# Performance work log

Measured on AMD Instinct MI355X. Metric: run time of the kernel, lower is better.

Reference implementation:

```python
import jax, jax.numpy as jnp
import numpy as np

H = 16  # attention heads


def setup_inputs() -> dict:
    key = jax.random.key(0)
    k0, k1, k2 = jax.random.split(key, 3)
    B, T, C = 2, 2048, 1024
    x = jax.random.normal(k0, (B, T, C), dtype=jnp.float32)
    W_attn = jax.random.normal(k1, (3 * C, C), dtype=jnp.float32) * 0.02
    W_proj = jax.random.normal(k2, (C, C), dtype=jnp.float32) * 0.02
    b_proj = jnp.zeros((C,), dtype=jnp.float32)
    return {"x": x, "W_attn": W_attn, "W_proj": W_proj, "b_proj": b_proj}


def reference(x, W_attn, W_proj, b_proj):
    # Eval-mode (dropout = identity), rotational_embeddings=False, flash=False path.
    B, T, C = x.shape
    d = C // H
    qkv = jnp.einsum('btc,fc->btf', x, W_attn)          # [B,T,3C] fused QKV proj
    q, k, v = jnp.split(qkv, 3, axis=-1)
    # [B,T,C] -> [B,H,T,d]
    q = q.reshape(B, T, H, d).transpose(0, 2, 1, 3)
    k = k.reshape(B, T, H, d).transpose(0, 2, 1, 3)
    v = v.reshape(B, T, H, d).transpose(0, 2, 1, 3)
    scale = 1.0 / np.sqrt(d).astype(np.float32)
    att = jnp.einsum('bhqd,bhkd->bhqk', q, k) * scale    # full TxT scores (no mask)
    att = jax.nn.softmax(att, axis=-1)
    y = jnp.einsum('bhqk,bhkd->bhqd', att, v)            # [B,H,T,d]
    y = y.transpose(0, 2, 1, 3).reshape(B, T, C)
    return jnp.einsum('btc,oc->bto', y, W_proj) + b_proj
```

## Files before the change

### kernel.cpp

```cpp
#include <hip/hip_runtime.h>
#include <hip/hip_bf16.h>
#include <stdint.h>

typedef __attribute__((ext_vector_type(8))) short bf16x8;
typedef __attribute__((ext_vector_type(4))) float f32x4;
typedef __attribute__((ext_vector_type(4))) unsigned u32x4;

#define MFMA16(A,B,C) __builtin_amdgcn_mfma_f32_16x16x32_bf16(A,B,C,0,0,0)


__device__ inline void gld_lds16(const __hip_bfloat16* g, __hip_bfloat16* l) {
  __builtin_amdgcn_global_load_lds(
      (const __attribute__((address_space(1))) void*)g,
      (__attribute__((address_space(3))) void*)l, 16, 0, 0);
}

__device__ inline void cvt_store8r(float4 u0, float4 u1,
                                   __hip_bfloat16* __restrict__ l) {
  __hip_bfloat162 t[4];
  t[0] = __float22bfloat162_rn(float2{u0.x, u0.y});
  t[1] = __float22bfloat162_rn(float2{u0.z, u0.w});
  t[2] = __float22bfloat162_rn(float2{u1.x, u1.y});
  t[3] = __float22bfloat162_rn(float2{u1.z, u1.w});
  *(int4*)l = *(const int4*)t;
}

__device__ inline void comb_store8r(int4 av, int4 bv, float rinv,
                                    __hip_bfloat16* __restrict__ l) {
  const __hip_bfloat162* ap = (const __hip_bfloat162*)&av;
  const __hip_bfloat162* bp = (const __hip_bfloat162*)&bv;
  __hip_bfloat162 t[4];
#pragma unroll
  for (int i = 0; i < 4; i++) {
    float2 fa = __bfloat1622float2(ap[i]);
    float2 fb = __bfloat1622float2(bp[i]);
    t[i] = __float22bfloat162_rn(float2{(fa.x + fb.x) * rinv,
                                        (fa.y + fb.y) * rinv});
  }
  *(int4*)l = *(const int4*)t;
}

__device__ inline unsigned pkbf(float a, float b) {
  __hip_bfloat162 t = __float22bfloat162_rn(float2{a, b});
  return *(unsigned*)&t;
}

__device__ inline void quad_mix(unsigned &a, unsigned &b) {
#if __has_builtin(__builtin_amdgcn_permlane32_swap) && __has_builtin(__builtin_amdgcn_permlane16_swap)
  auto r1 = __builtin_amdgcn_permlane32_swap(a, b, false, false);
  auto r2 = __builtin_amdgcn_permlane16_swap(r1[0], r1[1], false, false);
  a = r2[0];
  b = r2[1];
#else
  int lane = (int)(threadIdx.x & 63);
  int g = lane >> 4;
  int lm = lane & 15;
  int slo = (((g << 1) & 3) << 4) | lm;
  int shi = ((((g << 1) | 1) & 3) << 4) | lm;
  unsigned t0 = (unsigned)__shfl((int)a, slo, 64);
  unsigned t1 = (unsigned)__shfl((int)b, slo, 64);
  unsigned t2 = (unsigned)__shfl((int)a, shi, 64);
  unsigned t3 = (unsigned)__shfl((int)b, shi, 64);
  bool hi = g >= 2;
  unsigned na = hi ? t1 : t0;
  unsigned nb = hi ? t3 : t2;
  a = na;
  b = nb;
#endif
}

__global__ __launch_bounds__(256)
void gemm_qkv(const float* __restrict__ A,
              const float* __restrict__ B,
              __hip_bfloat16* __restrict__ C,
              __hip_bfloat16* __restrict__ vtg,
              int M, int N, int K)
{
  __shared__ __align__(16) __hip_bfloat16 As[128 * 32];
  __shared__ __align__(16) __hip_bfloat16 Bs[128 * 32];

  const int tid  = threadIdx.x;
  const int lane = tid & 63;
  const int w    = tid >> 6;
  const int lm   = lane & 15;
  const int g    = lane >> 4;

  const int bm = blockIdx.y * 128;
  const int bn = blockIdx.x * 128;
  const int rm = (w >> 1) * 64;
  const int cn = (w & 1) * 64;

  const int row0 = tid >> 2;
  const int kc   = (tid & 3) * 8;

  float4 pa[2][2], pb[2][2];
  auto ldtile = [&](int k0) {
#pragma unroll
    for (int p = 0; p < 2; p++) {
      const float* ga = A + (size_t)(bm + row0 + 64 * p) * K + k0 + kc;
      pa[p][0] = *(const float4*)ga;
      pa[p][1] = *(const float4*)(ga + 4);
      const float* gb = B + (size_t)(bn + row0 + 64 * p) * K + k0 + kc;
      pb[p][0] = *(const float4*)gb;
      pb[p][1] = *(const float4*)(gb + 4);
    }
  };

  const f32x4 fzero = {0.0f, 0.0f, 0.0f, 0.0f};
  f32x4 acc[4][4];
  for (int i = 0; i < 4; i++)
    for (int j = 0; j < 4; j++)
      acc[i][j] = fzero;

  ldtile(0);
  for (int k0 = 0; k0 < K; k0 += 32) {
#pragma unroll
    for (int p = 0; p < 2; p++) {
      int row = row0 + 64 * p;
      cvt_store8r(pa[p][0], pa[p][1], &As[row * 32 + kc]);
      cvt_store8r(pb[p][0], pb[p][1], &Bs[row * 32 + kc]);
    }
    __syncthreads();
    if (k0 + 32 < K) ldtile(k0 + 32);

    bf16x8 af[4], bfr[4];
#pragma unroll
    for (int i = 0; i < 4; i++)
      af[i] = *(const bf16x8*)&As[(rm + 16 * i + lm) * 32 + 8 * g];
#pragma unroll
    for (int j = 0; j < 4; j++)
      bfr[j] = *(const bf16x8*)&Bs[(cn + 16 * j + lm) * 32 + 8 * g];
#pragma unroll
    for (int i = 0; i < 4; i++)
#pragma unroll
      for (int j = 0; j < 4; j++)
        acc[i][j] = MFMA16(af[i], bfr[j], acc[i][j]);
    __syncthreads();
  }

  if (bn >= 2048) {
#pragma unroll
    for (int j = 0; j < 4; j++) {
      int colv = bn + cn + 16 * j + lm - 2048;
      int vh = colv >> 6, dd = colv & 63;
#pragma unroll
      for (int i = 0; i < 4; i++) {
        int m0 = bm + rm + 16 * i + 4 * g;
        int bb = m0 >> 11, t0 = m0 & 2047;
        __hip_bfloat16 t4[4];
#pragma unroll
        for (int r = 0; r < 4; r++) t4[r] = __float2bfloat16(acc[i][j][r]);
        *(int2*)&vtg[((size_t)(bb * 16 + vh) * 64 + dd) * 2048 + t0] =
            *(const int2*)t4;
      }
    }
    return;
  }

  const float qs = (bn < 1024) ? (0.125f * 1.4426950408889634f) : 1.0f;
#pragma unroll
  for (int j = 0; j < 4; j++) {
    int coln = bn + cn + 16 * j + lm;
#pragma unroll
    for (int i = 0; i < 4; i++) {
#pragma unroll
      for (int r = 0; r < 4; r++) {
        int rowm = bm + rm + 16 * i + 4 * g + r;
        C[(size_t)rowm * N + coln] = __float2bfloat16(acc[i][j][r] * qs);
      }
    }
  }
}

__global__ __launch_bounds__(256)
void gemm_out(const __hip_bfloat16* __restrict__ po,
              const float* __restrict__ pl,
              const float* __restrict__ Bw,
              const float* __restrict__ bias,
              float* __restrict__ out,
              int M, int N, int K)
{
  __shared__ __align__(16) __hip_bfloat16 As[128 * 32];
  __shared__ __align__(16) __hip_bfloat16 Bs[64 * 32];

  const int tid  = threadIdx.x;
  const int lane = tid & 63;
  const int w    = tid >> 6;
  const int lm   = lane & 15;
  const int g    = lane >> 4;

  const int bm = blockIdx.y * 128;
  const int bn = blockIdx.x * 64;
  const int rm = (w >> 1) * 64;
  const int cn = (w & 1) * 32;

  const int row0 = tid >> 2;
  const int kc   = (tid & 3) * 8;

  int4  qa[2], qb[2];
  float la[2], lb[2];
  float4 wb0, wb1;
  auto ldtile = [&](int k0) {
    const int h = k0 >> 6;
#pragma unroll
    for (int p = 0; p < 2; p++) {
      int m = bm + row0 + 64 * p;
      qa[p] = *(const int4*)(po + (size_t)m * 1024 + k0 + kc);
      qb[p] = *(const int4*)(po + (size_t)4096 * 1024 + (size_t)m * 1024 + k0 + kc);
      la[p] = pl[m * 16 + h];
      lb[p] = pl[4096 * 16 + m * 16 + h];
    }
    const float* gb = Bw + (size_t)(bn + row0) * K + k0 + kc;
    wb0 = *(const float4*)gb;
    wb1 = *(const float4*)(gb + 4);
  };

  const f32x4 fzero = {0.0f, 0.0f, 0.0f, 0.0f};
  f32x4 acc[4][2];
  for (int i = 0; i < 4; i++)
    for (int j = 0; j < 2; j++)
      acc[i][j] = fzero;

  ldtile(0);
  for (int k0 = 0; k0 < K; k0 += 32) {
#pragma unroll
    for (int p = 0; p < 2; p++)
      comb_store8r(qa[p], qb[p], 1.0f / (la[p] + lb[p]),
                   &As[(row0 + 64 * p) * 32 + kc]);
    cvt_store8r(wb0, wb1, &Bs[row0 * 32 + kc]);
    __syncthreads();
    if (k0 + 32 < K) ldtile(k0 + 32);

    bf16x8 af[4], bfr[2];
#pragma unroll
    for (int i = 0; i < 4; i++)
      af[i] = *(const bf16x8*)&As[(rm + 16 * i + lm) * 32 + 8 * g];
#pragma unroll
    for (int j = 0; j < 2; j++)
      bfr[j] = *(const bf16x8*)&Bs[(cn + 16 * j + lm) * 32 + 8 * g];
#pragma unroll
    for (int i = 0; i < 4; i++)
#pragma unroll
      for (int j = 0; j < 2; j++)
        acc[i][j] = MFMA16(af[i], bfr[j], acc[i][j]);
    __syncthreads();
  }

#pragma unroll
  for (int j = 0; j < 2; j++) {
    int coln = bn + cn + 16 * j + lm;
    float bv = bias[coln];
#pragma unroll
    for (int i = 0; i < 4; i++) {
#pragma unroll
      for (int r = 0; r < 4; r++) {
        int rowm = bm + rm + 16 * i + 4 * g + r;
        out[(size_t)rowm * N + coln] = acc[i][j][r] + bv;
      }
    }
  }
}

__global__ __launch_bounds__(256)
void mha(const __hip_bfloat16* __restrict__ qkv,
         const __hip_bfloat16* __restrict__ vtg,
         __hip_bfloat16* __restrict__ po,
         float* __restrict__ pl,
         int nsteps)
{
  const int T = 2048, F = 3072, Cc = 1024;
  const int bh = blockIdx.x;
  const int b  = bh >> 4, h = bh & 15;
  const int qb0 = blockIdx.y * 128;
  const int z   = blockIdx.z;
  const int kvb = z * 32 * nsteps;

  const int tid  = threadIdx.x;
  const int lane = tid & 63;
  const int w    = tid >> 6;
  const int lm   = lane & 15;
  const int g    = lane >> 4;

  __shared__ __align__(16) __hip_bfloat16 Ks[2][32 * 64];
  __shared__ __align__(16) __hip_bfloat16 Vs[2][64 * 32];

  const size_t rowbase = (size_t)b * T * F;
  const int hoff = h * 64;
  const __hip_bfloat16* Kbase = qkv + rowbase + 1024 + hoff;
  const __hip_bfloat16* Vtb   = vtg + (size_t)(b * 16 + h) * 64 * 2048;

  const int qw = qb0 + 32 * w;
  bf16x8 aq[2][2];
#pragma unroll
  for (int mt = 0; mt < 2; mt++)
#pragma unroll
    for (int e = 0; e < 2; e++)
      aq[mt][e] = *(const bf16x8*)
          &qkv[rowbase + (size_t)(qw + 16 * mt + lm) * F + hoff + 32 * e + 8 * g];

  const f32x4 fzero = {0.0f, 0.0f, 0.0f, 0.0f};
  f32x4 yacc[2][4];
  float lsum[2] = {0.0f, 0.0f};
#pragma unroll
  for (int mt = 0; mt < 2; mt++)
#pragma unroll
    for (int c = 0; c < 4; c++) yacc[mt][c] = fzero;

  const int r0  = tid >> 3;
  const int swK = (tid & 7) ^ (r0 & 7);
  const int vdd = tid >> 2;
  const int vk  = (tid & 3) ^ ((tid >> 3) & 3);
  const int sxK = lm & 7;
  const int sxV = (lm >> 1) & 3;

  gld_lds16(Kbase + (size_t)(kvb + r0) * F + swK * 8, &Ks[0][tid * 8]);
  gld_lds16(Vtb + (size_t)vdd * 2048 + kvb + vk * 8, &Vs[0][tid * 8]);

  for (int t = 0; t < nsteps; t++) {
    const int buf = t & 1;
    __syncthreads();
    if (t + 1 < nsteps) {
      const int kvn = kvb + (t + 1) * 32;
      gld_lds16(Kbase + (size_t)(kvn + r0) * F + swK * 8, &Ks[buf ^ 1][tid * 8]);
      gld_lds16(Vtb + (size_t)vdd * 2048 + kvn + vk * 8, &Vs[buf ^ 1][tid * 8]);
    }

    bf16x8 kf[2][2];
#pragma unroll
    for (int c2 = 0; c2 < 2; c2++) {
      kf[c2][0] = *(const bf16x8*)&Ks[buf][(16 * c2 + lm) * 64 + ((0 + g) ^ sxK) * 8];
      kf[c2][1] = *(const bf16x8*)&Ks[buf][(16 * c2 + lm) * 64 + ((4 + g) ^ sxK) * 8];
    }
#pragma unroll
    for (int mt = 0; mt < 2; mt++) {
      f32x4 st[2];
#pragma unroll
      for (int c2 = 0; c2 < 2; c2++) {
        st[c2] = MFMA16(kf[c2][0], aq[mt][0], fzero);
        st[c2] = MFMA16(kf[c2][1], aq[mt][1], st[c2]);
      }

      unsigned pkv[2][2];
#pragma unroll
      for (int c2 = 0; c2 < 2; c2++)
#pragma unroll
        for (int u = 0; u < 2; u++) {
          float p0 = __builtin_amdgcn_exp2f(st[c2][2 * u]);
          float p1 = __builtin_amdgcn_exp2f(st[c2][2 * u + 1]);
          lsum[mt] += p0 + p1;
          pkv[c2][u] = pkbf(p0, p1);
        }

      unsigned f0 = pkv[0][0], f2 = pkv[1][0];
      quad_mix(f0, f2);
      unsigned f1 = pkv[0][1], f3 = pkv[1][1];
      quad_mix(f1, f3);
      u32x4 fv = {f0, f1, f2, f3};
      bf16x8 ap = __builtin_bit_cast(bf16x8, fv);

#pragma unroll
      for (int c = 0; c < 4; c++) {
        bf16x8 bv = *(const bf16x8*)&Vs[buf][(16 * c + lm) * 32 + (g ^ sxV) * 8];
        yacc[mt][c] = MFMA16(ap, bv, yacc[mt][c]);
      }
    }
  }

  float lred[2];
#pragma unroll
  for (int mt = 0; mt < 2; mt++) {
    float ls = lsum[mt];
    ls += __shfl_xor(ls, 16);
    ls += __shfl_xor(ls, 32);
    lred[mt] = ls;
  }

  __hip_bfloat16* pz = po + (size_t)z * 4096 * 1024;
  float* plz = pl + (size_t)z * 4096 * 16;
#pragma unroll
  for (int mt = 0; mt < 2; mt++) {
#pragma unroll
    for (int c = 0; c < 4; c++)
#pragma unroll
      for (int r = 0; r < 4; r++) {
        int qrow = qw + 16 * mt + 4 * g + r;
        pz[(size_t)(b * T + qrow) * Cc + hoff + 16 * c + lm] =
            __float2bfloat16(yacc[mt][c][r]);
      }
    if (lane < 16)
      plz[(b * T + qw + 16 * mt + lane) * 16 + h] = lred[mt];
  }
}

extern "C" void kernel_launch(void* const* d_in, const int* in_sizes, int n_in,
                              void* d_out, int out_size, void* d_ws, size_t ws_size,
                              hipStream_t stream)
{
  const float* x  = (const float*)d_in[0];
  const float* Wa = (const float*)d_in[1];
  const float* Wp = (const float*)d_in[2];
  const float* bp = (const float*)d_in[3];
  float* out = (float*)d_out;

  const int BT = 4096, C = 1024, F3 = 3072;
  char* ws = (char*)d_ws;
  __hip_bfloat16* qkv  = (__hip_bfloat16*)ws;
  __hip_bfloat16* vtg  = (__hip_bfloat16*)(ws + 25165824);
  __hip_bfloat16* Opar = (__hip_bfloat16*)(ws + 33554432);
  float*          lpar = (float*)(ws + 50331648);

  gemm_qkv<<<dim3(F3 / 128, BT / 128), 256, 0, stream>>>(x, Wa, qkv, vtg,
                                                         BT, F3, C);
  mha<<<dim3(32, 16, 2), 256, 0, stream>>>(qkv, vtg, Opar, lpar, 32);
  gemm_out<<<dim3(C / 64, BT / 128), 256, 0, stream>>>(Opar, lpar, Wp, bp, out,
                                                       BT, C, C);
}
```

Baseline: 209.2 us.

## Double-buffer GEMM LDS tiles, split attention KV four ways, compact QK buffer

Both GEMMs now use double-buffered LDS with a single barrier per k-step, so staging the next tile overlaps the MFMA work on the current one. The QKV GEMM gets launch bounds asking for three blocks per SM. The attention kernel splits the KV range into 4 chunks instead of 2 to launch more blocks, and the output GEMM uses 64x64 tiles and merges four partial outputs and sums. The QK intermediate is stored with a 2048 row stride instead of 3072 because V is already written transposed separately. In exchange, the output GEMM reads more partial data and the larger partial buffers raise memory traffic.

```diff
diff --git a/kernel.cpp b/kernel.cpp
--- a/kernel.cpp
+++ b/kernel.cpp
@@ -25,17 +25,19 @@
   *(int4*)l = *(const int4*)t;
 }
 
-__device__ inline void comb_store8r(int4 av, int4 bv, float rinv,
-                                    __hip_bfloat16* __restrict__ l) {
-  const __hip_bfloat162* ap = (const __hip_bfloat162*)&av;
-  const __hip_bfloat162* bp = (const __hip_bfloat162*)&bv;
+__device__ inline void comb_store8r4(const int4* q, float rinv,
+                                     __hip_bfloat16* __restrict__ l) {
   __hip_bfloat162 t[4];
 #pragma unroll
   for (int i = 0; i < 4; i++) {
-    float2 fa = __bfloat1622float2(ap[i]);
-    float2 fb = __bfloat1622float2(bp[i]);
-    t[i] = __float22bfloat162_rn(float2{(fa.x + fb.x) * rinv,
-                                        (fa.y + fb.y) * rinv});
+    float2 s = {0.0f, 0.0f};
+#pragma unroll
+    for (int z = 0; z < 4; z++) {
+      __hip_bfloat162 h2 = ((const __hip_bfloat162*)&q[z])[i];
+      float2 f = __bfloat1622float2(h2);
+      s.x += f.x; s.y += f.y;
+    }
+    t[i] = __float22bfloat162_rn(float2{s.x * rinv, s.y * rinv});
   }
   *(int4*)l = *(const int4*)t;
 }
@@ -69,15 +71,15 @@
 #endif
 }
 
-__global__ __launch_bounds__(256)
+__global__ __launch_bounds__(256, 3)
 void gemm_qkv(const float* __restrict__ A,
               const float* __restrict__ B,
-              __hip_bfloat16* __restrict__ C,
+              __hip_bfloat16* __restrict__ qk,
               __hip_bfloat16* __restrict__ vtg,
               int M, int N, int K)
 {
-  __shared__ __align__(16) __hip_bfloat16 As[128 * 32];
-  __shared__ __align__(16) __hip_bfloat16 Bs[128 * 32];
+  __shared__ __align__(16) __hip_bfloat16 As[2][128 * 32];
+  __shared__ __align__(16) __hip_bfloat16 Bs[2][128 * 32];
 
   const int tid  = threadIdx.x;
   const int lane = tid & 63;
@@ -105,6 +107,14 @@
       pb[p][1] = *(const float4*)(gb + 4);
     }
   };
+  auto sttile = [&](int s) {
+#pragma unroll
+    for (int p = 0; p < 2; p++) {
+      int row = row0 + 64 * p;
+      cvt_store8r(pa[p][0], pa[p][1], &As[s][row * 32 + kc]);
+      cvt_store8r(pb[p][0], pb[p][1], &Bs[s][row * 32 + kc]);
+    }
+  };
 
   const f32x4 fzero = {0.0f, 0.0f, 0.0f, 0.0f};
   f32x4 acc[4][4];
@@ -113,29 +123,29 @@
       acc[i][j] = fzero;
 
   ldtile(0);
-  for (int k0 = 0; k0 < K; k0 += 32) {
-#pragma unroll
-    for (int p = 0; p < 2; p++) {
-      int row = row0 + 64 * p;
-      cvt_store8r(pa[p][0], pa[p][1], &As[row * 32 + kc]);
-      cvt_store8r(pb[p][0], pb[p][1], &Bs[row * 32 + kc]);
-    }
+  sttile(0);
+  ldtile(32);
+
+  for (int t = 0; t < 32; t++) {
+    const int rb = t & 1;
     __syncthreads();
-    if (k0 + 32 < K) ldtile(k0 + 32);
+    if (t + 1 < 32) {
+      sttile(rb ^ 1);
+      if (t + 2 < 32) ldtile((t + 2) * 32);
+    }
 
     bf16x8 af[4], bfr[4];
 #pragma unroll
     for (int i = 0; i < 4; i++)
-      af[i] = *(const bf16x8*)&As[(rm + 16 * i + lm) * 32 + 8 * g];
+      af[i] = *(const bf16x8*)&As[rb][(rm + 16 * i + lm) * 32 + 8 * g];
 #pragma unroll
     for (int j = 0; j < 4; j++)
-      bfr[j] = *(const bf16x8*)&Bs[(cn + 16 * j + lm) * 32 + 8 * g];
+      bfr[j] = *(const bf16x8*)&Bs[rb][(cn + 16 * j + lm) * 32 + 8 * g];
 #pragma unroll
     for (int i = 0; i < 4; i++)
 #pragma unroll
       for (int j = 0; j < 4; j++)
         acc[i][j] = MFMA16(af[i], bfr[j], acc[i][j]);
-    __syncthreads();
   }
 
   if (bn >= 2048) {
@@ -166,7 +176,7 @@
 #pragma unroll
       for (int r = 0; r < 4; r++) {
         int rowm = bm + rm + 16 * i + 4 * g + r;
-        C[(size_t)rowm * N + coln] = __float2bfloat16(acc[i][j][r] * qs);
+        qk[(size_t)rowm * 2048 + coln] = __float2bfloat16(acc[i][j][r] * qs);
       }
     }
   }
@@ -180,8 +190,8 @@
               float* __restrict__ out,
               int M, int N, int K)
 {
-  __shared__ __align__(16) __hip_bfloat16 As[128 * 32];
-  __shared__ __align__(16) __hip_bfloat16 Bs[64 * 32];
+  __shared__ __align__(16) __hip_bfloat16 As[2][64 * 32];
+  __shared__ __align__(16) __hip_bfloat16 Bs[2][64 * 32];
 
   const int tid  = threadIdx.x;
   const int lane = tid & 63;
@@ -189,61 +199,66 @@
   const int lm   = lane & 15;
   const int g    = lane >> 4;
 
-  const int bm = blockIdx.y * 128;
+  const int bm = blockIdx.y * 64;
   const int bn = blockIdx.x * 64;
-  const int rm = (w >> 1) * 64;
+  const int rm = (w >> 1) * 32;
   const int cn = (w & 1) * 32;
 
   const int row0 = tid >> 2;
   const int kc   = (tid & 3) * 8;
 
-  int4  qa[2], qb[2];
-  float la[2], lb[2];
+  int4  qa[4];
+  float rinv;
   float4 wb0, wb1;
   auto ldtile = [&](int k0) {
     const int h = k0 >> 6;
-#pragma unroll
-    for (int p = 0; p < 2; p++) {
-      int m = bm + row0 + 64 * p;
-      qa[p] = *(const int4*)(po + (size_t)m * 1024 + k0 + kc);
-      qb[p] = *(const int4*)(po + (size_t)4096 * 1024 + (size_t)m * 1024 + k0 + kc);
-      la[p] = pl[m * 16 + h];
-      lb[p] = pl[4096 * 16 + m * 16 + h];
-    }
+    int m = bm + row0;
+    float ls = 0.0f;
+#pragma unroll
+    for (int z = 0; z < 4; z++) {
+      qa[z] = *(const int4*)(po + (size_t)z * 4096 * 1024 + (size_t)m * 1024 + k0 + kc);
+      ls += pl[z * 4096 * 16 + m * 16 + h];
+    }
+    rinv = 1.0f / ls;
     const float* gb = Bw + (size_t)(bn + row0) * K + k0 + kc;
     wb0 = *(const float4*)gb;
     wb1 = *(const float4*)(gb + 4);
   };
+  auto sttile = [&](int s) {
+    comb_store8r4(qa, rinv, &As[s][row0 * 32 + kc]);
+    cvt_store8r(wb0, wb1, &Bs[s][row0 * 32 + kc]);
+  };
 
   const f32x4 fzero = {0.0f, 0.0f, 0.0f, 0.0f};
-  f32x4 acc[4][2];
-  for (int i = 0; i < 4; i++)
+  f32x4 acc[2][2];
+  for (int i = 0; i < 2; i++)
     for (int j = 0; j < 2; j++)
       acc[i][j] = fzero;
 
   ldtile(0);
-  for (int k0 = 0; k0 < K; k0 += 32) {
-#pragma unroll
-    for (int p = 0; p < 2; p++)
-      comb_store8r(qa[p], qb[p], 1.0f / (la[p] + lb[p]),
-                   &As[(row0 + 64 * p) * 32 + kc]);
-    cvt_store8r(wb0, wb1, &Bs[row0 * 32 + kc]);
+  sttile(0);
+  ldtile(32);
+
+  for (int t = 0; t < 32; t++) {
+    const int rb = t & 1;
     __syncthreads();
-    if (k0 + 32 < K) ldtile(k0 + 32);
-
-    bf16x8 af[4], bfr[2];
-#pragma unroll
-    for (int i = 0; i < 4; i++)
-      af[i] = *(const bf16x8*)&As[(rm + 16 * i + lm) * 32 + 8 * g];
+    if (t + 1 < 32) {
+      sttile(rb ^ 1);
+      if (t + 2 < 32) ldtile((t + 2) * 32);
+    }
+
+    bf16x8 af[2], bfr[2];
+#pragma unroll
+    for (int i = 0; i < 2; i++)
+      af[i] = *(const bf16x8*)&As[rb][(rm + 16 * i + lm) * 32 + 8 * g];
 #pragma unroll
     for (int j = 0; j < 2; j++)
-      bfr[j] = *(const bf16x8*)&Bs[(cn + 16 * j + lm) * 32 + 8 * g];
-#pragma unroll
-    for (int i = 0; i < 4; i++)
+      bfr[j] = *(const bf16x8*)&Bs[rb][(cn + 16 * j + lm) * 32 + 8 * g];
+#pragma unroll
+    for (int i = 0; i < 2; i++)
 #pragma unroll
       for (int j = 0; j < 2; j++)
         acc[i][j] = MFMA16(af[i], bfr[j], acc[i][j]);
-    __syncthreads();
   }
 
 #pragma unroll
@@ -251,7 +266,7 @@
     int coln = bn + cn + 16 * j + lm;
     float bv = bias[coln];
 #pragma unroll
-    for (int i = 0; i < 4; i++) {
+    for (int i = 0; i < 2; i++) {
 #pragma unroll
       for (int r = 0; r < 4; r++) {
         int rowm = bm + rm + 16 * i + 4 * g + r;
@@ -262,13 +277,13 @@
 }
 
 __global__ __launch_bounds__(256)
-void mha(const __hip_bfloat16* __restrict__ qkv,
+void mha(const __hip_bfloat16* __restrict__ qk,
          const __hip_bfloat16* __restrict__ vtg,
          __hip_bfloat16* __restrict__ po,
          float* __restrict__ pl,
          int nsteps)
 {
-  const int T = 2048, F = 3072, Cc = 1024;
+  const int T = 2048, Cc = 1024;
   const int bh = blockIdx.x;
   const int b  = bh >> 4, h = bh & 15;
   const int qb0 = blockIdx.y * 128;
@@ -284,9 +299,9 @@
   __shared__ __align__(16) __hip_bfloat16 Ks[2][32 * 64];
   __shared__ __align__(16) __hip_bfloat16 Vs[2][64 * 32];
 
-  const size_t rowbase = (size_t)b * T * F;
+  const size_t rowbase = (size_t)b * T * 2048;
   const int hoff = h * 64;
-  const __hip_bfloat16* Kbase = qkv + rowbase + 1024 + hoff;
+  const __hip_bfloat16* Kbase = qk + rowbase + 1024 + hoff;
   const __hip_bfloat16* Vtb   = vtg + (size_t)(b * 16 + h) * 64 * 2048;
 
   const int qw = qb0 + 32 * w;
@@ -296,7 +311,7 @@
 #pragma unroll
     for (int e = 0; e < 2; e++)
       aq[mt][e] = *(const bf16x8*)
-          &qkv[rowbase + (size_t)(qw + 16 * mt + lm) * F + hoff + 32 * e + 8 * g];
+          &qk[rowbase + (size_t)(qw + 16 * mt + lm) * 2048 + hoff + 32 * e + 8 * g];
 
   const f32x4 fzero = {0.0f, 0.0f, 0.0f, 0.0f};
   f32x4 yacc[2][4];
@@ -313,7 +328,7 @@
   const int sxK = lm & 7;
   const int sxV = (lm >> 1) & 3;
 
-  gld_lds16(Kbase + (size_t)(kvb + r0) * F + swK * 8, &Ks[0][tid * 8]);
+  gld_lds16(Kbase + (size_t)(kvb + r0) * 2048 + swK * 8, &Ks[0][tid * 8]);
   gld_lds16(Vtb + (size_t)vdd * 2048 + kvb + vk * 8, &Vs[0][tid * 8]);
 
   for (int t = 0; t < nsteps; t++) {
@@ -321,7 +336,7 @@
     __syncthreads();
     if (t + 1 < nsteps) {
       const int kvn = kvb + (t + 1) * 32;
-      gld_lds16(Kbase + (size_t)(kvn + r0) * F + swK * 8, &Ks[buf ^ 1][tid * 8]);
+      gld_lds16(Kbase + (size_t)(kvn + r0) * 2048 + swK * 8, &Ks[buf ^ 1][tid * 8]);
       gld_lds16(Vtb + (size_t)vdd * 2048 + kvn + vk * 8, &Vs[buf ^ 1][tid * 8]);
     }
 
@@ -404,14 +419,14 @@
 
   const int BT = 4096, C = 1024, F3 = 3072;
   char* ws = (char*)d_ws;
-  __hip_bfloat16* qkv  = (__hip_bfloat16*)ws;
-  __hip_bfloat16* vtg  = (__hip_bfloat16*)(ws + 25165824);
-  __hip_bfloat16* Opar = (__hip_bfloat16*)(ws + 33554432);
-  float*          lpar = (float*)(ws + 50331648);
-
-  gemm_qkv<<<dim3(F3 / 128, BT / 128), 256, 0, stream>>>(x, Wa, qkv, vtg,
+  __hip_bfloat16* qk   = (__hip_bfloat16*)ws;
+  __hip_bfloat16* vtg  = (__hip_bfloat16*)(ws + 16777216);
+  __hip_bfloat16* Opar = (__hip_bfloat16*)(ws + 25165824);
+  float*          lpar = (float*)(ws + 58720256);
+
+  gemm_qkv<<<dim3(F3 / 128, BT / 128), 256, 0, stream>>>(x, Wa, qk, vtg,
                                                          BT, F3, C);
-  mha<<<dim3(32, 16, 2), 256, 0, stream>>>(qkv, vtg, Opar, lpar, 32);
-  gemm_out<<<dim3(C / 64, BT / 128), 256, 0, stream>>>(Opar, lpar, Wp, bp, out,
-                                                       BT, C, C);
-}
+  mha<<<dim3(32, 16, 4), 256, 0, stream>>>(qk, vtg, Opar, lpar, 16);
+  gemm_out<<<dim3(C / 64, BT / 64), 256, 0, stream>>>(Opar, lpar, Wp, bp, out,
+                                                      BT, C, C);
+}
```

After: 236.6 us. 1.13x slower.
